# Kernel optimization log

Hardware: AMD Instinct MI355X
Metric: run time of the kernel (lower is better)

The kernel has to match this reference:

```python
import jax, jax.numpy as jnp
import numpy as np

N_NODES = 2048
EMBED = 256
STATE = 128
HID = 256
N_ACT = 256
TEAMS = 8
PAIR_F = 14


def setup_inputs() -> dict:
    key = jax.random.key(0)
    ks = jax.random.split(key, 12)
    B, T = 16, 32
    node_embeddings = jax.random.normal(ks[0], (N_NODES, EMBED), jnp.float32)
    states = jax.random.normal(ks[1], (B, T, STATE), jnp.float32)
    pair_features = jax.random.normal(ks[2], (B, T, N_ACT, PAIR_F), jnp.float32)
    proc_action_indices = jax.random.randint(ks[3], (N_ACT,), 0, N_NODES)
    in_dim = EMBED * 4 + PAIR_F
    s = lambda k, sh, fan: jax.random.normal(k, sh, jnp.float32) / np.sqrt(fan)
    return {
        "node_embeddings": node_embeddings,
        "states": states,
        "pair_features": pair_features,
        "proc_action_indices": proc_action_indices,
        "team_table": jax.random.normal(ks[4], (TEAMS, EMBED), jnp.float32),
        "Ws": s(ks[5], (STATE, EMBED), STATE),
        "bs": jnp.zeros((EMBED,), jnp.float32),
        "W1": s(ks[6], (in_dim, HID), in_dim),
        "b1": jnp.zeros((HID,), jnp.float32),
        "W2": s(ks[7], (HID, HID), HID),
        "b2": jnp.zeros((HID,), jnp.float32),
        "W3": s(ks[8], (HID, 1), HID),
        "b3": jnp.zeros((1,), jnp.float32),
    }


def reference(node_embeddings, states, pair_features, proc_action_indices,
              team_table, Ws, bs, W1, b1, W2, b2, W3, b3):
    B, T, A, F = pair_features.shape
    team_ids = jnp.arange(A) % TEAMS  # registered buffer
    # [A, E] gathered / per-action embeddings
    proc_emb = node_embeddings[proc_action_indices]          # [A, E]
    team_emb = team_table[team_ids]                          # [A, E]
    global_emb = jnp.mean(node_embeddings, axis=0)           # [E]
    state_emb = jax.nn.relu(states @ Ws + bs)                # [B, T, E]
    # broadcast + concat -> [B, T, A, 4E + F]
    bT = (B, T, A)
    scorer_input = jnp.concatenate([
        jnp.broadcast_to(proc_emb[None, None], bT + (proc_emb.shape[-1],)),
        jnp.broadcast_to(team_emb[None, None], bT + (team_emb.shape[-1],)),
        jnp.broadcast_to(global_emb[None, None, None], bT + (global_emb.shape[-1],)),
        jnp.broadcast_to(state_emb[:, :, None], bT + (state_emb.shape[-1],)),
        pair_features,
    ], axis=-1)
    h = jax.nn.relu(scorer_input @ W1 + b1)
    h = jax.nn.relu(h @ W2 + b2)
    scores = (h @ W3 + b3)[..., 0]  # [B, T, A]
    return scores[:, :, None, :]    # [B, T, 1, A]
```

## Files before the change

kernel.cpp:

```cpp
#include <hip/hip_runtime.h>
#include <hip/hip_bf16.h>

#define N_NODES 2048
#define EMBED 256
#define STATE 128
#define HID 256
#define N_ACT 256
#define TEAMS 8
#define PAIR_F 14
#define BT_TOTAL 512
#define M_TOTAL (BT_TOTAL * N_ACT)

typedef _Float16 f16_t;
typedef _Float16 f16x8 __attribute__((ext_vector_type(8)));
typedef _Float16 f16x4 __attribute__((ext_vector_type(4)));
typedef _Float16 f16x2 __attribute__((ext_vector_type(2)));
typedef float f32x4 __attribute__((ext_vector_type(4)));

__device__ __forceinline__ size_t reord_idx(int k, int n, int KB) {
    return (size_t)(((n >> 4) * KB + (k >> 5)) * 4 + ((k >> 3) & 3)) * 128 +
           (size_t)(n & 15) * 8 + (k & 7);
}

__device__ __forceinline__ size_t par_idx(int a, int n) {
    return (size_t)(a >> 4) * 4096 + (size_t)(n >> 2) * 64 + (a & 15) * 4 + (n & 3);
}

__device__ __forceinline__ f16x8 gather8(const float* __restrict__ W, int k0, int n, int ld) {
    f16x8 r;
#pragma unroll
    for (int j = 0; j < 8; ++j) r[j] = (f16_t)W[(size_t)(k0 + j) * ld + n];
    return r;
}

__device__ __forceinline__ f16x2 pk_relu(f16x2 x) {
    f16x2 r;
    asm("v_pk_max_f16 %0, %1, %2" : "=v"(r) : "v"(x), "v"(f16x2{(_Float16)0, (_Float16)0}));
    return r;
}

__device__ __forceinline__ f16x2 cvt_pk(float lo, float hi) {
    return __builtin_bit_cast(f16x2, __builtin_amdgcn_cvt_pkrtz(lo, hi));
}

__global__ void k_prep(const float* __restrict__ ne, const int* __restrict__ idx,
                       const float* __restrict__ team, const float* __restrict__ states,
                       const float* __restrict__ Ws, const float* __restrict__ W1,
                       const float* __restrict__ W2, const float* __restrict__ pf,
                       float* __restrict__ gpart, f16_t* __restrict__ vecs,
                       f16_t* __restrict__ W1abT, f16_t* __restrict__ W1cT,
                       f16_t* __restrict__ W1dT, f16_t* __restrict__ WsT,
                       f16_t* __restrict__ W2s, f16_t* __restrict__ w1pt,
                       f16_t* __restrict__ states_h, f16_t* __restrict__ pf16) {
    int bid = blockIdx.x;
    if (bid < 64) {
        int t = threadIdx.x;
        float s = 0.f;
        const float* base = ne + (size_t)bid * 32 * EMBED + t;
#pragma unroll
        for (int i = 0; i < 32; ++i) s += base[(size_t)i * EMBED];
        gpart[bid * EMBED + t] = s;
        return;
    }
    int u = (bid - 64) * 256 + threadIdx.x;
    if (u < 16384) {
        int a = u >> 6, e = (u & 63) * 8;
        f16x8 r;
        if (e < 256) {
            const float* src = ne + (size_t)idx[a] * EMBED + e;
#pragma unroll
            for (int j = 0; j < 8; ++j) r[j] = (f16_t)src[j];
        } else {
            const float* src = team + (size_t)(a % TEAMS) * EMBED + (e - 256);
#pragma unroll
            for (int j = 0; j < 8; ++j) r[j] = (f16_t)src[j];
        }
        *(f16x8*)(vecs + (size_t)u * 8) = r;
        return;
    }
    u -= 16384;
    if (u < 16384) {
        int c = u & 15, q = (u >> 4) & 3, kb = (u >> 6) & 15, g = u >> 10;
        *(f16x8*)(W1abT + (size_t)u * 8) = gather8(W1, kb * 32 + q * 8, g * 16 + c, HID);
        return;
    }
    u -= 16384;
    if (u < 8192) {
        int c = u & 15, q = (u >> 4) & 3, kb = (u >> 6) & 7, g = u >> 9;
        *(f16x8*)(W1cT + (size_t)u * 8) = gather8(W1, 512 + kb * 32 + q * 8, g * 16 + c, HID);
        return;
    }
    u -= 8192;
    if (u < 8192) {
        int c = u & 15, q = (u >> 4) & 3, kb = (u >> 6) & 7, g = u >> 9;
        *(f16x8*)(W1dT + (size_t)u * 8) = gather8(W1, 768 + kb * 32 + q * 8, g * 16 + c, HID);
        return;
    }
    u -= 8192;
    if (u < 4096) {
        int c = u & 15, q = (u >> 4) & 3, kb = (u >> 6) & 3, g = u >> 8;
        *(f16x8*)(WsT + (size_t)u * 8) = gather8(Ws, kb * 32 + q * 8, g * 16 + c, EMBED);
        return;
    }
    u -= 4096;
    if (u < 8192) {
        int c = u & 15, q = (u >> 4) & 3, kb = (u >> 6) & 7, g = u >> 9;
        *(f16x8*)(W2s + (size_t)u * 8) = gather8(W2, kb * 32 + q * 8, g * 16 + c, HID);
        return;
    }
    u -= 8192;
    if (u < 1024) {
        int c = u & 15, q = (u >> 4) & 3, g = u >> 6;
        int n = g * 16 + c, k0 = q * 8;
        f16x8 r;
#pragma unroll
        for (int j = 0; j < 8; ++j) {
            int k = k0 + j;
            r[j] = (f16_t)((k < PAIR_F) ? W1[(size_t)(1024 + k) * HID + n] : 0.f);
        }
        *(f16x8*)(w1pt + (size_t)u * 8) = r;
        return;
    }
    u -= 1024;
    if (u < 8192) {
        const float* src = states + (size_t)u * 8;
        f16x8 r;
#pragma unroll
        for (int j = 0; j < 8; ++j) r[j] = (f16_t)src[j];
        *(f16x8*)(states_h + (size_t)u * 8) = r;
        return;
    }
    u -= 8192;
    if (u < 262144) {
        int m = u >> 1, h = u & 1;
        const float* row = pf + (size_t)m * PAIR_F;
        f16x8 r;
        if (h == 0) {
#pragma unroll
            for (int j = 0; j < 4; ++j) {
                float2 v = *(const float2*)(row + j * 2);
                r[j * 2] = (f16_t)v.x; r[j * 2 + 1] = (f16_t)v.y;
            }
        } else {
#pragma unroll
            for (int j = 0; j < 3; ++j) {
                float2 v = *(const float2*)(row + 8 + j * 2);
                r[j * 2] = (f16_t)v.x; r[j * 2 + 1] = (f16_t)v.y;
            }
            r[6] = (f16_t)0.f; r[7] = (f16_t)0.f;
        }
        *(f16x8*)(pf16 + (size_t)u * 8) = r;
    }
}

__global__ __launch_bounds__(256, 4) void k_pp(
    const f16_t* __restrict__ states_h, const f16_t* __restrict__ WsT,
    const float* __restrict__ bs, const f16_t* __restrict__ W1dT,
    const f16_t* __restrict__ vecs, const f16_t* __restrict__ W1abT,
    const f16_t* __restrict__ W1cT, const float* __restrict__ gpart,
    const float* __restrict__ b1, f16_t* __restrict__ paR,
    f16_t* __restrict__ pbt_h) {
    __shared__ __align__(16) f16_t se[32 * 256];
    __shared__ __align__(16) f16_t gml[256];
    const int tid = threadIdx.x;
    const int wid = tid >> 6, lane = tid & 63;
    const int c = lane & 15, q = lane >> 4;
    int bid = blockIdx.x;

    if (bid >= 16) {
        {
            float s = 0.f;
#pragma unroll 8
            for (int p = 0; p < 64; ++p) s += gpart[p * EMBED + tid];
            gml[tid] = (f16_t)(s * (1.0f / N_NODES));
        }
        __syncthreads();
        int b = bid - 16;
        const int m0 = (b >> 2) * 32, n0 = (b & 3) * 64;
        const int n = n0 + wid * 16 + c;
        const int g = n >> 4;
        f32x4 acc[2] = {f32x4{0,0,0,0}, f32x4{0,0,0,0}};
        for (int ks = 0; ks < 16; ++ks) {
            f16x8 bf = *(const f16x8*)(W1abT + (size_t)((g * 16 + ks) * 4 + q) * 128 + c * 8);
#pragma unroll
            for (int mi = 0; mi < 2; ++mi) {
                f16x8 af = *(const f16x8*)(vecs + (size_t)(m0 + mi * 16 + c) * 512 + ks * 32 + q * 8);
                acc[mi] = __builtin_amdgcn_mfma_f32_16x16x32_f16(af, bf, acc[mi], 0, 0, 0);
            }
        }
#pragma unroll
        for (int ks = 0; ks < 8; ++ks) {
            f16x8 bf = *(const f16x8*)(W1cT + (size_t)((g * 8 + ks) * 4 + q) * 128 + c * 8);
            f16x8 af = *(const f16x8*)(gml + ks * 32 + q * 8);
#pragma unroll
            for (int mi = 0; mi < 2; ++mi)
                acc[mi] = __builtin_amdgcn_mfma_f32_16x16x32_f16(af, bf, acc[mi], 0, 0, 0);
        }
        float b1v = b1[n];
#pragma unroll
        for (int mi = 0; mi < 2; ++mi)
#pragma unroll
            for (int j = 0; j < 4; ++j) {
                int a = m0 + mi * 16 + q * 4 + j;
                paR[par_idx(a, n)] = (f16_t)(acc[mi][j] + b1v);
            }
        return;
    }

    const int bt0 = bid * 32;
    f32x4 acc[2][4];
#pragma unroll
    for (int mi = 0; mi < 2; ++mi)
#pragma unroll
        for (int ni = 0; ni < 4; ++ni) acc[mi][ni] = f32x4{0, 0, 0, 0};
#pragma unroll
    for (int ks = 0; ks < 4; ++ks) {
        f16x8 bh[4];
#pragma unroll
        for (int ni = 0; ni < 4; ++ni) {
            int g = wid * 4 + ni;
            bh[ni] = *(const f16x8*)(WsT + (size_t)((g * 4 + ks) * 4 + q) * 128 + c * 8);
        }
#pragma unroll
        for (int mi = 0; mi < 2; ++mi) {
            f16x8 af = *(const f16x8*)(states_h + (size_t)(bt0 + mi * 16 + c) * STATE + ks * 32 + q * 8);
#pragma unroll
            for (int ni = 0; ni < 4; ++ni)
                acc[mi][ni] = __builtin_amdgcn_mfma_f32_16x16x32_f16(af, bh[ni], acc[mi][ni], 0, 0, 0);
        }
    }
#pragma unroll
    for (int mi = 0; mi < 2; ++mi)
#pragma unroll
        for (int ni = 0; ni < 4; ++ni) {
            float bsv = bs[wid * 64 + ni * 16 + c];
#pragma unroll
            for (int j = 0; j < 4; ++j) {
                int m = mi * 16 + q * 4 + j;
                int n = wid * 64 + ni * 16 + c;
                se[m * 256 + (n ^ ((m & 7) << 3))] = (f16_t)fmaxf(acc[mi][ni][j] + bsv, 0.f);
            }
        }
#pragma unroll
    for (int mi = 0; mi < 2; ++mi)
#pragma unroll
        for (int ni = 0; ni < 4; ++ni) acc[mi][ni] = f32x4{0, 0, 0, 0};
    __syncthreads();
#pragma unroll
    for (int ks = 0; ks < 8; ++ks) {
        f16x8 bh[4];
#pragma unroll
        for (int ni = 0; ni < 4; ++ni) {
            int g = wid * 4 + ni;
            bh[ni] = *(const f16x8*)(W1dT + (size_t)((g * 8 + ks) * 4 + q) * 128 + c * 8);
        }
#pragma unroll
        for (int mi = 0; mi < 2; ++mi) {
            int m = mi * 16 + c;
            f16x8 ah = *(const f16x8*)(&se[m * 256 + ((ks * 32 + q * 8) ^ ((m & 7) << 3))]);
#pragma unroll
            for (int ni = 0; ni < 4; ++ni)
                acc[mi][ni] = __builtin_amdgcn_mfma_f32_16x16x32_f16(ah, bh[ni], acc[mi][ni], 0, 0, 0);
        }
    }
#pragma unroll
    for (int mi = 0; mi < 2; ++mi)
#pragma unroll
        for (int ni = 0; ni < 4; ++ni)
#pragma unroll
            for (int j = 0; j < 4; ++j)
                pbt_h[(size_t)(bt0 + mi * 16 + q * 4 + j) * HID + wid * 64 + ni * 16 + c] =
                    (f16_t)acc[mi][ni][j];
}

__global__ __launch_bounds__(512, 4) void k_main(
    const f16_t* __restrict__ pf16, const f16_t* __restrict__ paR,
    const f16_t* __restrict__ pbt, const f16_t* __restrict__ w2s,
    const f16_t* __restrict__ w1pt, const float* __restrict__ b2,
    const float* __restrict__ W3, const float* __restrict__ b3,
    float* __restrict__ out) {
    __shared__ __align__(16) f16_t Ah[128 * 256];
    __shared__ float red[4][128];

    const int tid = threadIdx.x;
    const int wid = tid >> 6, lane = tid & 63;
    const int wr = wid >> 2, wc = wid & 3;
    const int c = lane & 15, q = lane >> 4;

    const int r0 = blockIdx.x * 128;
    const int bt = r0 >> 8;
    const int a0 = r0 & 255;

    f32x4 acc[16];
#pragma unroll
    for (int i = 0; i < 16; ++i) acc[i] = f32x4{0, 0, 0, 0};

    f16x4 pbtv[4];
#pragma unroll
    for (int nf = 0; nf < 4; ++nf)
        pbtv[nf] = *(const f16x4*)(pbt + (size_t)bt * HID + wc * 64 + nf * 16 + q * 4);

    f16x8 af[4];
#pragma unroll
    for (int nf = 0; nf < 4; ++nf) {
        int g = wc * 4 + nf;
        af[nf] = *(const f16x8*)(w1pt + (size_t)(g * 4 + q) * 128 + c * 8);
    }

    f16x4 pavA[4], pavB[4];
    {
        int n0 = wc * 64 + 0 * 16 + q * 4;
#pragma unroll
        for (int mf = 0; mf < 4; ++mf)
            pavA[mf] = *(const f16x4*)(paR + (size_t)((a0 >> 4) + wr * 4 + mf) * 4096 +
                                       (size_t)(n0 >> 2) * 64 + c * 4);
    }

#pragma unroll
    for (int mf = 0; mf < 4; ++mf) {
        int m = wr * 64 + mf * 16 + c;
        f16x8 bf;
        if (q < 2) bf = *(const f16x8*)(pf16 + (size_t)(r0 + m) * 16 + q * 8);
        else bf = f16x8{(_Float16)0, (_Float16)0, (_Float16)0, (_Float16)0,
                        (_Float16)0, (_Float16)0, (_Float16)0, (_Float16)0};
        __builtin_amdgcn_s_setprio(1);
#pragma unroll
        for (int nf = 0; nf < 4; ++nf)
            acc[nf * 4 + mf] = __builtin_amdgcn_mfma_f32_16x16x32_f16(af[nf], bf, acc[nf * 4 + mf], 0, 0, 0);
        __builtin_amdgcn_s_setprio(0);
    }

#pragma unroll
    for (int nf = 0; nf < 4; ++nf) {
        if (nf < 3) {
            int n1 = wc * 64 + (nf + 1) * 16 + q * 4;
#pragma unroll
            for (int mf = 0; mf < 4; ++mf)
                pavB[mf] = *(const f16x4*)(paR + (size_t)((a0 >> 4) + wr * 4 + mf) * 4096 +
                                           (size_t)(n1 >> 2) * 64 + c * 4);
        }
        int n0 = wc * 64 + nf * 16 + q * 4;
        f16x2 pb01 = {pbtv[nf][0], pbtv[nf][1]}, pb23 = {pbtv[nf][2], pbtv[nf][3]};
#pragma unroll
        for (int mf = 0; mf < 4; ++mf) {
            int m = wr * 64 + mf * 16 + c;
            f16x2 pa01 = {pavA[mf][0], pavA[mf][1]}, pa23 = {pavA[mf][2], pavA[mf][3]};
            f32x4 a = acc[nf * 4 + mf];
            f16x2 h01 = cvt_pk(a[0], a[1]);
            f16x2 h23 = cvt_pk(a[2], a[3]);
            h01 = pk_relu(h01 + pa01 + pb01);
            h23 = pk_relu(h23 + pa23 + pb23);
            f16x4 hv = __builtin_shufflevector(h01, h23, 0, 1, 2, 3);
            *(f16x4*)(&Ah[m * 256 + (n0 ^ ((m & 7) << 3))]) = hv;
        }
#pragma unroll
        for (int mf = 0; mf < 4; ++mf) pavA[mf] = pavB[mf];
    }

#pragma unroll
    for (int i = 0; i < 16; ++i) acc[i] = f32x4{0, 0, 0, 0};

    f16x8 bh[4];
#pragma unroll
    for (int ni = 0; ni < 4; ++ni) {
        int g = wc * 4 + ni;
        bh[ni] = *(const f16x8*)(w2s + (size_t)((g * 8 + 0) * 4 + q) * 128 + c * 8);
    }

    __syncthreads();

#pragma unroll
    for (int ks = 0; ks < 8; ++ks) {
        f16x8 bhn[4];
        if (ks < 7) {
#pragma unroll
            for (int ni = 0; ni < 4; ++ni) {
                int g = wc * 4 + ni;
                bhn[ni] = *(const f16x8*)(w2s + (size_t)((g * 8 + ks + 1) * 4 + q) * 128 + c * 8);
            }
        }
        f16x8 ahA, ahB;
        {
            int m = wr * 64 + 0 * 16 + c;
            ahA = *(const f16x8*)(&Ah[m * 256 + ((ks * 32 + q * 8) ^ ((m & 7) << 3))]);
        }
        __builtin_amdgcn_s_setprio(1);
#pragma unroll
        for (int mi = 0; mi < 4; ++mi) {
            if (mi < 3) {
                int m1 = wr * 64 + (mi + 1) * 16 + c;
                ahB = *(const f16x8*)(&Ah[m1 * 256 + ((ks * 32 + q * 8) ^ ((m1 & 7) << 3))]);
            }
#pragma unroll
            for (int ni = 0; ni < 4; ++ni)
                acc[mi * 4 + ni] = __builtin_amdgcn_mfma_f32_16x16x32_f16(ahA, bh[ni], acc[mi * 4 + ni], 0, 0, 0);
            ahA = ahB;
        }
        __builtin_amdgcn_s_setprio(0);
#pragma unroll
        for (int ni = 0; ni < 4; ++ni) bh[ni] = bhn[ni];
    }

    float p[4][4];
#pragma unroll
    for (int mi = 0; mi < 4; ++mi)
#pragma unroll
        for (int j = 0; j < 4; ++j) p[mi][j] = 0.f;
#pragma unroll
    for (int ni = 0; ni < 4; ++ni) {
        int n = wc * 64 + ni * 16 + c;
        float b2v = b2[n];
        float w3v = W3[n];
#pragma unroll
        for (int mi = 0; mi < 4; ++mi)
#pragma unroll
            for (int j = 0; j < 4; ++j)
                p[mi][j] = fmaf(fmaxf(acc[mi * 4 + ni][j] + b2v, 0.f), w3v, p[mi][j]);
    }
#pragma unroll
    for (int off = 1; off < 16; off <<= 1)
#pragma unroll
        for (int mi = 0; mi < 4; ++mi)
#pragma unroll
            for (int j = 0; j < 4; ++j) p[mi][j] += __shfl_xor(p[mi][j], off, 64);

    if (c == 0) {
#pragma unroll
        for (int mi = 0; mi < 4; ++mi)
#pragma unroll
            for (int j = 0; j < 4; ++j) red[wc][wr * 64 + mi * 16 + q * 4 + j] = p[mi][j];
    }
    __syncthreads();

    if (tid < 128) {
        out[(size_t)r0 + tid] = red[0][tid] + red[1][tid] + red[2][tid] + red[3][tid] + b3[0];
    }
}

extern "C" void kernel_launch(void* const* d_in, const int* in_sizes, int n_in,
                              void* d_out, int out_size, void* d_ws, size_t ws_size,
                              hipStream_t stream) {
    (void)in_sizes; (void)n_in; (void)out_size; (void)ws_size;
    const float* ne     = (const float*)d_in[0];
    const float* states = (const float*)d_in[1];
    const float* pf     = (const float*)d_in[2];
    const int*   idx    = (const int*)d_in[3];
    const float* team   = (const float*)d_in[4];
    const float* Ws     = (const float*)d_in[5];
    const float* bs     = (const float*)d_in[6];
    const float* W1     = (const float*)d_in[7];
    const float* b1     = (const float*)d_in[8];
    const float* W2     = (const float*)d_in[9];
    const float* b2     = (const float*)d_in[10];
    const float* W3     = (const float*)d_in[11];
    const float* b3     = (const float*)d_in[12];
    float* out = (float*)d_out;

    char* ws = (char*)d_ws;
    float* gpart    = (float*)(ws + 0);
    f16_t* vecs     = (f16_t*)(ws + 65536);
    f16_t* W1abT    = (f16_t*)(ws + 327680);
    f16_t* W1cT     = (f16_t*)(ws + 589824);
    f16_t* W1dT     = (f16_t*)(ws + 720896);
    f16_t* WsT      = (f16_t*)(ws + 851968);
    f16_t* W2s      = (f16_t*)(ws + 917504);
    f16_t* w1pt     = (f16_t*)(ws + 1048576);
    f16_t* states_h = (f16_t*)(ws + 1064960);
    f16_t* paR      = (f16_t*)(ws + 1196032);
    f16_t* pbt_h    = (f16_t*)(ws + 1327104);
    f16_t* pf16     = (f16_t*)(ws + 1589248);

    k_prep<<<64 + 1300, 256, 0, stream>>>(ne, idx, team, states, Ws, W1, W2, pf,
                                          gpart, vecs, W1abT, W1cT, W1dT, WsT, W2s,
                                          w1pt, states_h, pf16);
    k_pp<<<48, 256, 0, stream>>>(states_h, WsT, bs, W1dT, vecs, W1abT, W1cT,
                                 gpart, b1, paR, pbt_h);
    k_main<<<M_TOTAL / 128, 512, 0, stream>>>(pf16, paR, pbt_h, W2s, w1pt, b2, W3, b3, out);
}
```

Baseline: 42.93 us.

## Fuse prep and projection kernels into one launch reading fp32 inputs directly

Merges the prep and per-action/per-state projection kernels into a single kernel. The projection blocks now read fp32 embeddings, states and weights directly and convert inline, instead of using pre-converted fp16 buffers. Each pa block computes the global mean over all nodes itself. This removes a kernel launch and intermediate workspace traffic, at the cost of redundant mean reduction and uncoalesced weight gathers on the critical path.

Result: slower. 80.93 us (+88.5%).

```diff
diff --git a/kernel.cpp b/kernel.cpp
--- a/kernel.cpp
+++ b/kernel.cpp
@@ -17,11 +17,6 @@
 typedef _Float16 f16x2 __attribute__((ext_vector_type(2)));
 typedef float f32x4 __attribute__((ext_vector_type(4)));
 
-__device__ __forceinline__ size_t reord_idx(int k, int n, int KB) {
-    return (size_t)(((n >> 4) * KB + (k >> 5)) * 4 + ((k >> 3) & 3)) * 128 +
-           (size_t)(n & 15) * 8 + (k & 7);
-}
-
 __device__ __forceinline__ size_t par_idx(int a, int n) {
     return (size_t)(a >> 4) * 4096 + (size_t)(n >> 2) * 64 + (a & 15) * 4 + (n & 3);
 }
@@ -30,6 +25,14 @@
     f16x8 r;
 #pragma unroll
     for (int j = 0; j < 8; ++j) r[j] = (f16_t)W[(size_t)(k0 + j) * ld + n];
+    return r;
+}
+
+__device__ __forceinline__ f16x8 load8_f32(const float* __restrict__ p) {
+    float4 v0 = *(const float4*)p, v1 = *(const float4*)(p + 4);
+    f16x8 r;
+    r[0] = (f16_t)v0.x; r[1] = (f16_t)v0.y; r[2] = (f16_t)v0.z; r[3] = (f16_t)v0.w;
+    r[4] = (f16_t)v1.x; r[5] = (f16_t)v1.y; r[6] = (f16_t)v1.z; r[7] = (f16_t)v1.w;
     return r;
 }
 
@@ -43,123 +46,15 @@
     return __builtin_bit_cast(f16x2, __builtin_amdgcn_cvt_pkrtz(lo, hi));
 }
 
-__global__ void k_prep(const float* __restrict__ ne, const int* __restrict__ idx,
-                       const float* __restrict__ team, const float* __restrict__ states,
-                       const float* __restrict__ Ws, const float* __restrict__ W1,
-                       const float* __restrict__ W2, const float* __restrict__ pf,
-                       float* __restrict__ gpart, f16_t* __restrict__ vecs,
-                       f16_t* __restrict__ W1abT, f16_t* __restrict__ W1cT,
-                       f16_t* __restrict__ W1dT, f16_t* __restrict__ WsT,
-                       f16_t* __restrict__ W2s, f16_t* __restrict__ w1pt,
-                       f16_t* __restrict__ states_h, f16_t* __restrict__ pf16) {
-    int bid = blockIdx.x;
-    if (bid < 64) {
-        int t = threadIdx.x;
-        float s = 0.f;
-        const float* base = ne + (size_t)bid * 32 * EMBED + t;
-#pragma unroll
-        for (int i = 0; i < 32; ++i) s += base[(size_t)i * EMBED];
-        gpart[bid * EMBED + t] = s;
-        return;
-    }
-    int u = (bid - 64) * 256 + threadIdx.x;
-    if (u < 16384) {
-        int a = u >> 6, e = (u & 63) * 8;
-        f16x8 r;
-        if (e < 256) {
-            const float* src = ne + (size_t)idx[a] * EMBED + e;
-#pragma unroll
-            for (int j = 0; j < 8; ++j) r[j] = (f16_t)src[j];
-        } else {
-            const float* src = team + (size_t)(a % TEAMS) * EMBED + (e - 256);
-#pragma unroll
-            for (int j = 0; j < 8; ++j) r[j] = (f16_t)src[j];
-        }
-        *(f16x8*)(vecs + (size_t)u * 8) = r;
-        return;
-    }
-    u -= 16384;
-    if (u < 16384) {
-        int c = u & 15, q = (u >> 4) & 3, kb = (u >> 6) & 15, g = u >> 10;
-        *(f16x8*)(W1abT + (size_t)u * 8) = gather8(W1, kb * 32 + q * 8, g * 16 + c, HID);
-        return;
-    }
-    u -= 16384;
-    if (u < 8192) {
-        int c = u & 15, q = (u >> 4) & 3, kb = (u >> 6) & 7, g = u >> 9;
-        *(f16x8*)(W1cT + (size_t)u * 8) = gather8(W1, 512 + kb * 32 + q * 8, g * 16 + c, HID);
-        return;
-    }
-    u -= 8192;
-    if (u < 8192) {
-        int c = u & 15, q = (u >> 4) & 3, kb = (u >> 6) & 7, g = u >> 9;
-        *(f16x8*)(W1dT + (size_t)u * 8) = gather8(W1, 768 + kb * 32 + q * 8, g * 16 + c, HID);
-        return;
-    }
-    u -= 8192;
-    if (u < 4096) {
-        int c = u & 15, q = (u >> 4) & 3, kb = (u >> 6) & 3, g = u >> 8;
-        *(f16x8*)(WsT + (size_t)u * 8) = gather8(Ws, kb * 32 + q * 8, g * 16 + c, EMBED);
-        return;
-    }
-    u -= 4096;
-    if (u < 8192) {
-        int c = u & 15, q = (u >> 4) & 3, kb = (u >> 6) & 7, g = u >> 9;
-        *(f16x8*)(W2s + (size_t)u * 8) = gather8(W2, kb * 32 + q * 8, g * 16 + c, HID);
-        return;
-    }
-    u -= 8192;
-    if (u < 1024) {
-        int c = u & 15, q = (u >> 4) & 3, g = u >> 6;
-        int n = g * 16 + c, k0 = q * 8;
-        f16x8 r;
-#pragma unroll
-        for (int j = 0; j < 8; ++j) {
-            int k = k0 + j;
-            r[j] = (f16_t)((k < PAIR_F) ? W1[(size_t)(1024 + k) * HID + n] : 0.f);
-        }
-        *(f16x8*)(w1pt + (size_t)u * 8) = r;
-        return;
-    }
-    u -= 1024;
-    if (u < 8192) {
-        const float* src = states + (size_t)u * 8;
-        f16x8 r;
-#pragma unroll
-        for (int j = 0; j < 8; ++j) r[j] = (f16_t)src[j];
-        *(f16x8*)(states_h + (size_t)u * 8) = r;
-        return;
-    }
-    u -= 8192;
-    if (u < 262144) {
-        int m = u >> 1, h = u & 1;
-        const float* row = pf + (size_t)m * PAIR_F;
-        f16x8 r;
-        if (h == 0) {
-#pragma unroll
-            for (int j = 0; j < 4; ++j) {
-                float2 v = *(const float2*)(row + j * 2);
-                r[j * 2] = (f16_t)v.x; r[j * 2 + 1] = (f16_t)v.y;
-            }
-        } else {
-#pragma unroll
-            for (int j = 0; j < 3; ++j) {
-                float2 v = *(const float2*)(row + 8 + j * 2);
-                r[j * 2] = (f16_t)v.x; r[j * 2 + 1] = (f16_t)v.y;
-            }
-            r[6] = (f16_t)0.f; r[7] = (f16_t)0.f;
-        }
-        *(f16x8*)(pf16 + (size_t)u * 8) = r;
-    }
-}
-
-__global__ __launch_bounds__(256, 4) void k_pp(
-    const f16_t* __restrict__ states_h, const f16_t* __restrict__ WsT,
-    const float* __restrict__ bs, const f16_t* __restrict__ W1dT,
-    const f16_t* __restrict__ vecs, const f16_t* __restrict__ W1abT,
-    const f16_t* __restrict__ W1cT, const float* __restrict__ gpart,
-    const float* __restrict__ b1, f16_t* __restrict__ paR,
-    f16_t* __restrict__ pbt_h) {
+__global__ __launch_bounds__(256, 4) void k_all(
+    const float* __restrict__ ne, const int* __restrict__ idx,
+    const float* __restrict__ team, const float* __restrict__ states,
+    const float* __restrict__ Ws, const float* __restrict__ W1,
+    const float* __restrict__ W2, const float* __restrict__ pf,
+    const float* __restrict__ bs, const float* __restrict__ b1,
+    f16_t* __restrict__ W2s, f16_t* __restrict__ w1pt,
+    f16_t* __restrict__ paR, f16_t* __restrict__ pbt_h,
+    f16_t* __restrict__ pf16) {
     __shared__ __align__(16) f16_t se[32 * 256];
     __shared__ __align__(16) f16_t gml[256];
     const int tid = threadIdx.x;
@@ -167,110 +62,166 @@
     const int c = lane & 15, q = lane >> 4;
     int bid = blockIdx.x;
 
-    if (bid >= 16) {
-        {
-            float s = 0.f;
-#pragma unroll 8
-            for (int p = 0; p < 64; ++p) s += gpart[p * EMBED + tid];
-            gml[tid] = (f16_t)(s * (1.0f / N_NODES));
-        }
+    if (bid < 48) {
+        if (bid >= 16) {
+            {
+                float s0 = 0, s1 = 0, s2 = 0, s3 = 0, s4 = 0, s5 = 0, s6 = 0, s7 = 0;
+                const float* col = ne + tid;
+                for (int r = 0; r < N_NODES; r += 8) {
+                    s0 += col[(size_t)(r + 0) * EMBED]; s1 += col[(size_t)(r + 1) * EMBED];
+                    s2 += col[(size_t)(r + 2) * EMBED]; s3 += col[(size_t)(r + 3) * EMBED];
+                    s4 += col[(size_t)(r + 4) * EMBED]; s5 += col[(size_t)(r + 5) * EMBED];
+                    s6 += col[(size_t)(r + 6) * EMBED]; s7 += col[(size_t)(r + 7) * EMBED];
+                }
+                float s = ((s0 + s1) + (s2 + s3)) + ((s4 + s5) + (s6 + s7));
+                gml[tid] = (f16_t)(s * (1.0f / N_NODES));
+            }
+            __syncthreads();
+            int b = bid - 16;
+            const int m0 = (b >> 2) * 32, n0 = (b & 3) * 64;
+            const int n = n0 + wid * 16 + c;
+            f32x4 acc[2] = {f32x4{0, 0, 0, 0}, f32x4{0, 0, 0, 0}};
+            const float* neb[2];
+            const float* tmb[2];
+#pragma unroll
+            for (int mi = 0; mi < 2; ++mi) {
+                int m = m0 + mi * 16 + c;
+                neb[mi] = ne + (size_t)idx[m] * EMBED;
+                tmb[mi] = team + (size_t)(m % TEAMS) * EMBED;
+            }
+#pragma unroll
+            for (int ks = 0; ks < 16; ++ks) {
+                f16x8 bf = gather8(W1, ks * 32 + q * 8, n, HID);
+#pragma unroll
+                for (int mi = 0; mi < 2; ++mi) {
+                    int e0 = ks * 32 + q * 8;
+                    const float* src = (ks < 8) ? (neb[mi] + e0) : (tmb[mi] + (e0 - 256));
+                    f16x8 af = load8_f32(src);
+                    acc[mi] = __builtin_amdgcn_mfma_f32_16x16x32_f16(af, bf, acc[mi], 0, 0, 0);
+                }
+            }
+#pragma unroll
+            for (int ks = 0; ks < 8; ++ks) {
+                f16x8 bf = gather8(W1, 512 + ks * 32 + q * 8, n, HID);
+                f16x8 af = *(const f16x8*)(gml + ks * 32 + q * 8);
+#pragma unroll
+                for (int mi = 0; mi < 2; ++mi)
+                    acc[mi] = __builtin_amdgcn_mfma_f32_16x16x32_f16(af, bf, acc[mi], 0, 0, 0);
+            }
+            float b1v = b1[n];
+#pragma unroll
+            for (int mi = 0; mi < 2; ++mi)
+#pragma unroll
+                for (int j = 0; j < 4; ++j) {
+                    int a = m0 + mi * 16 + q * 4 + j;
+                    paR[par_idx(a, n)] = (f16_t)(acc[mi][j] + b1v);
+                }
+            return;
+        }
+
+        const int bt0 = bid * 32;
+        f32x4 acc[2][4];
+#pragma unroll
+        for (int mi = 0; mi < 2; ++mi)
+#pragma unroll
+            for (int ni = 0; ni < 4; ++ni) acc[mi][ni] = f32x4{0, 0, 0, 0};
+#pragma unroll
+        for (int ks = 0; ks < 4; ++ks) {
+            f16x8 bh[4];
+#pragma unroll
+            for (int ni = 0; ni < 4; ++ni)
+                bh[ni] = gather8(Ws, ks * 32 + q * 8, (wid * 4 + ni) * 16 + c, EMBED);
+#pragma unroll
+            for (int mi = 0; mi < 2; ++mi) {
+                f16x8 af = load8_f32(states + (size_t)(bt0 + mi * 16 + c) * STATE + ks * 32 + q * 8);
+#pragma unroll
+                for (int ni = 0; ni < 4; ++ni)
+                    acc[mi][ni] = __builtin_amdgcn_mfma_f32_16x16x32_f16(af, bh[ni], acc[mi][ni], 0, 0, 0);
+            }
+        }
+#pragma unroll
+        for (int mi = 0; mi < 2; ++mi)
+#pragma unroll
+            for (int ni = 0; ni < 4; ++ni) {
+                float bsv = bs[wid * 64 + ni * 16 + c];
+#pragma unroll
+                for (int j = 0; j < 4; ++j) {
+                    int m = mi * 16 + q * 4 + j;
+                    int n = wid * 64 + ni * 16 + c;
+                    se[m * 256 + (n ^ ((m & 7) << 3))] = (f16_t)fmaxf(acc[mi][ni][j] + bsv, 0.f);
+                }
+            }
+#pragma unroll
+        for (int mi = 0; mi < 2; ++mi)
+#pragma unroll
+            for (int ni = 0; ni < 4; ++ni) acc[mi][ni] = f32x4{0, 0, 0, 0};
         __syncthreads();
-        int b = bid - 16;
-        const int m0 = (b >> 2) * 32, n0 = (b & 3) * 64;
-        const int n = n0 + wid * 16 + c;
-        const int g = n >> 4;
-        f32x4 acc[2] = {f32x4{0,0,0,0}, f32x4{0,0,0,0}};
-        for (int ks = 0; ks < 16; ++ks) {
-            f16x8 bf = *(const f16x8*)(W1abT + (size_t)((g * 16 + ks) * 4 + q) * 128 + c * 8);
+#pragma unroll
+        for (int ks = 0; ks < 8; ++ks) {
+            f16x8 bh[4];
+#pragma unroll
+            for (int ni = 0; ni < 4; ++ni)
+                bh[ni] = gather8(W1, 768 + ks * 32 + q * 8, (wid * 4 + ni) * 16 + c, HID);
 #pragma unroll
             for (int mi = 0; mi < 2; ++mi) {
-                f16x8 af = *(const f16x8*)(vecs + (size_t)(m0 + mi * 16 + c) * 512 + ks * 32 + q * 8);
-                acc[mi] = __builtin_amdgcn_mfma_f32_16x16x32_f16(af, bf, acc[mi], 0, 0, 0);
-            }
-        }
-#pragma unroll
-        for (int ks = 0; ks < 8; ++ks) {
-            f16x8 bf = *(const f16x8*)(W1cT + (size_t)((g * 8 + ks) * 4 + q) * 128 + c * 8);
-            f16x8 af = *(const f16x8*)(gml + ks * 32 + q * 8);
-#pragma unroll
-            for (int mi = 0; mi < 2; ++mi)
-                acc[mi] = __builtin_amdgcn_mfma_f32_16x16x32_f16(af, bf, acc[mi], 0, 0, 0);
-        }
-        float b1v = b1[n];
+                int m = mi * 16 + c;
+                f16x8 ah = *(const f16x8*)(&se[m * 256 + ((ks * 32 + q * 8) ^ ((m & 7) << 3))]);
+#pragma unroll
+                for (int ni = 0; ni < 4; ++ni)
+                    acc[mi][ni] = __builtin_amdgcn_mfma_f32_16x16x32_f16(ah, bh[ni], acc[mi][ni], 0, 0, 0);
+            }
+        }
 #pragma unroll
         for (int mi = 0; mi < 2; ++mi)
 #pragma unroll
+            for (int ni = 0; ni < 4; ++ni)
+#pragma unroll
+                for (int j = 0; j < 4; ++j)
+                    pbt_h[(size_t)(bt0 + mi * 16 + q * 4 + j) * HID + wid * 64 + ni * 16 + c] =
+                        (f16_t)acc[mi][ni][j];
+        return;
+    }
+
+    int u = (bid - 48) * 256 + tid;
+    if (u < 262144) {
+        int m = u >> 1, h = u & 1;
+        const float* row = pf + (size_t)m * PAIR_F;
+        f16x8 r;
+        if (h == 0) {
+#pragma unroll
             for (int j = 0; j < 4; ++j) {
-                int a = m0 + mi * 16 + q * 4 + j;
-                paR[par_idx(a, n)] = (f16_t)(acc[mi][j] + b1v);
-            }
+                float2 v = *(const float2*)(row + j * 2);
+                r[j * 2] = (f16_t)v.x; r[j * 2 + 1] = (f16_t)v.y;
+            }
+        } else {
+#pragma unroll
+            for (int j = 0; j < 3; ++j) {
+                float2 v = *(const float2*)(row + 8 + j * 2);
+                r[j * 2] = (f16_t)v.x; r[j * 2 + 1] = (f16_t)v.y;
+            }
+            r[6] = (f16_t)0.f; r[7] = (f16_t)0.f;
+        }
+        *(f16x8*)(pf16 + (size_t)u * 8) = r;
         return;
     }
-
-    const int bt0 = bid * 32;
-    f32x4 acc[2][4];
-#pragma unroll
-    for (int mi = 0; mi < 2; ++mi)
-#pragma unroll
-        for (int ni = 0; ni < 4; ++ni) acc[mi][ni] = f32x4{0, 0, 0, 0};
-#pragma unroll
-    for (int ks = 0; ks < 4; ++ks) {
-        f16x8 bh[4];
-#pragma unroll
-        for (int ni = 0; ni < 4; ++ni) {
-            int g = wid * 4 + ni;
-            bh[ni] = *(const f16x8*)(WsT + (size_t)((g * 4 + ks) * 4 + q) * 128 + c * 8);
-        }
-#pragma unroll
-        for (int mi = 0; mi < 2; ++mi) {
-            f16x8 af = *(const f16x8*)(states_h + (size_t)(bt0 + mi * 16 + c) * STATE + ks * 32 + q * 8);
-#pragma unroll
-            for (int ni = 0; ni < 4; ++ni)
-                acc[mi][ni] = __builtin_amdgcn_mfma_f32_16x16x32_f16(af, bh[ni], acc[mi][ni], 0, 0, 0);
-        }
-    }
-#pragma unroll
-    for (int mi = 0; mi < 2; ++mi)
-#pragma unroll
-        for (int ni = 0; ni < 4; ++ni) {
-            float bsv = bs[wid * 64 + ni * 16 + c];
-#pragma unroll
-            for (int j = 0; j < 4; ++j) {
-                int m = mi * 16 + q * 4 + j;
-                int n = wid * 64 + ni * 16 + c;
-                se[m * 256 + (n ^ ((m & 7) << 3))] = (f16_t)fmaxf(acc[mi][ni][j] + bsv, 0.f);
-            }
-        }
-#pragma unroll
-    for (int mi = 0; mi < 2; ++mi)
-#pragma unroll
-        for (int ni = 0; ni < 4; ++ni) acc[mi][ni] = f32x4{0, 0, 0, 0};
-    __syncthreads();
-#pragma unroll
-    for (int ks = 0; ks < 8; ++ks) {
-        f16x8 bh[4];
-#pragma unroll
-        for (int ni = 0; ni < 4; ++ni) {
-            int g = wid * 4 + ni;
-            bh[ni] = *(const f16x8*)(W1dT + (size_t)((g * 8 + ks) * 4 + q) * 128 + c * 8);
-        }
-#pragma unroll
-        for (int mi = 0; mi < 2; ++mi) {
-            int m = mi * 16 + c;
-            f16x8 ah = *(const f16x8*)(&se[m * 256 + ((ks * 32 + q * 8) ^ ((m & 7) << 3))]);
-#pragma unroll
-            for (int ni = 0; ni < 4; ++ni)
-                acc[mi][ni] = __builtin_amdgcn_mfma_f32_16x16x32_f16(ah, bh[ni], acc[mi][ni], 0, 0, 0);
-        }
-    }
-#pragma unroll
-    for (int mi = 0; mi < 2; ++mi)
-#pragma unroll
-        for (int ni = 0; ni < 4; ++ni)
-#pragma unroll
-            for (int j = 0; j < 4; ++j)
-                pbt_h[(size_t)(bt0 + mi * 16 + q * 4 + j) * HID + wid * 64 + ni * 16 + c] =
-                    (f16_t)acc[mi][ni][j];
+    u -= 262144;
+    if (u < 8192) {
+        int c2 = u & 15, q2 = (u >> 4) & 3, kb = (u >> 6) & 7, g = u >> 9;
+        *(f16x8*)(W2s + (size_t)u * 8) = gather8(W2, kb * 32 + q2 * 8, g * 16 + c2, HID);
+        return;
+    }
+    u -= 8192;
+    if (u < 1024) {
+        int c2 = u & 15, q2 = (u >> 4) & 3, g = u >> 6;
+        int n = g * 16 + c2, k0 = q2 * 8;
+        f16x8 r;
+#pragma unroll
+        for (int j = 0; j < 8; ++j) {
+            int k = k0 + j;
+            r[j] = (f16_t)((k < PAIR_F) ? W1[(size_t)(1024 + k) * HID + n] : 0.f);
+        }
+        *(f16x8*)(w1pt + (size_t)u * 8) = r;
+    }
 }
 
 __global__ __launch_bounds__(512, 4) void k_main(
@@ -457,23 +408,13 @@
     float* out = (float*)d_out;
 
     char* ws = (char*)d_ws;
-    float* gpart    = (float*)(ws + 0);
-    f16_t* vecs     = (f16_t*)(ws + 65536);
-    f16_t* W1abT    = (f16_t*)(ws + 327680);
-    f16_t* W1cT     = (f16_t*)(ws + 589824);
-    f16_t* W1dT     = (f16_t*)(ws + 720896);
-    f16_t* WsT      = (f16_t*)(ws + 851968);
-    f16_t* W2s      = (f16_t*)(ws + 917504);
-    f16_t* w1pt     = (f16_t*)(ws + 1048576);
-    f16_t* states_h = (f16_t*)(ws + 1064960);
-    f16_t* paR      = (f16_t*)(ws + 1196032);
-    f16_t* pbt_h    = (f16_t*)(ws + 1327104);
-    f16_t* pf16     = (f16_t*)(ws + 1589248);
-
-    k_prep<<<64 + 1300, 256, 0, stream>>>(ne, idx, team, states, Ws, W1, W2, pf,
-                                          gpart, vecs, W1abT, W1cT, W1dT, WsT, W2s,
-                                          w1pt, states_h, pf16);
-    k_pp<<<48, 256, 0, stream>>>(states_h, WsT, bs, W1dT, vecs, W1abT, W1cT,
-                                 gpart, b1, paR, pbt_h);
+    f16_t* W2s   = (f16_t*)(ws + 0);
+    f16_t* w1pt  = (f16_t*)(ws + 131072);
+    f16_t* paR   = (f16_t*)(ws + 147456);
+    f16_t* pbt_h = (f16_t*)(ws + 278528);
+    f16_t* pf16  = (f16_t*)(ws + 540672);
+
+    k_all<<<48 + 1060, 256, 0, stream>>>(ne, idx, team, states, Ws, W1, W2, pf,
+                                         bs, b1, W2s, w1pt, paR, pbt_h, pf16);
     k_main<<<M_TOTAL / 128, 512, 0, stream>>>(pf16, paR, pbt_h, W2s, w1pt, b2, W3, b3, out);
 }
```

## Move pair-feature and W2 conversion into the precompute kernel to overlap work

Applied to the files above, without the earlier changes.

Splits the preparation work differently across the two pre-kernels. The first kernel now only does what the small precompute GEMMs depend on (global sum, gathers, W1/Ws transposes, states conversion). The large pair-feature f16 conversion and the W2/w1p repacking move into the second kernel, where they run alongside the 48 MFMA precompute blocks. This shortens the critical path before the precompute GEMMs and fills the GPU during the otherwise tiny 48-block launch. In exchange, the second kernel carries a larger shared-memory and register footprint for all its blocks.

Result: no change. 42.78 us, median of 3 (-0.3%).

```diff
diff --git a/kernel.cpp b/kernel.cpp
--- a/kernel.cpp
+++ b/kernel.cpp
@@ -17,11 +17,6 @@
 typedef _Float16 f16x2 __attribute__((ext_vector_type(2)));
 typedef float f32x4 __attribute__((ext_vector_type(4)));
 
-__device__ __forceinline__ size_t reord_idx(int k, int n, int KB) {
-    return (size_t)(((n >> 4) * KB + (k >> 5)) * 4 + ((k >> 3) & 3)) * 128 +
-           (size_t)(n & 15) * 8 + (k & 7);
-}
-
 __device__ __forceinline__ size_t par_idx(int a, int n) {
     return (size_t)(a >> 4) * 4096 + (size_t)(n >> 2) * 64 + (a & 15) * 4 + (n & 3);
 }
@@ -43,15 +38,13 @@
     return __builtin_bit_cast(f16x2, __builtin_amdgcn_cvt_pkrtz(lo, hi));
 }
 
-__global__ void k_prep(const float* __restrict__ ne, const int* __restrict__ idx,
-                       const float* __restrict__ team, const float* __restrict__ states,
-                       const float* __restrict__ Ws, const float* __restrict__ W1,
-                       const float* __restrict__ W2, const float* __restrict__ pf,
-                       float* __restrict__ gpart, f16_t* __restrict__ vecs,
-                       f16_t* __restrict__ W1abT, f16_t* __restrict__ W1cT,
-                       f16_t* __restrict__ W1dT, f16_t* __restrict__ WsT,
-                       f16_t* __restrict__ W2s, f16_t* __restrict__ w1pt,
-                       f16_t* __restrict__ states_h, f16_t* __restrict__ pf16) {
+__global__ void k_prepA(const float* __restrict__ ne, const int* __restrict__ idx,
+                        const float* __restrict__ team, const float* __restrict__ states,
+                        const float* __restrict__ Ws, const float* __restrict__ W1,
+                        float* __restrict__ gpart, f16_t* __restrict__ vecs,
+                        f16_t* __restrict__ W1abT, f16_t* __restrict__ W1cT,
+                        f16_t* __restrict__ W1dT, f16_t* __restrict__ WsT,
+                        f16_t* __restrict__ states_h) {
     int bid = blockIdx.x;
     if (bid < 64) {
         int t = threadIdx.x;
@@ -104,62 +97,24 @@
     }
     u -= 4096;
     if (u < 8192) {
-        int c = u & 15, q = (u >> 4) & 3, kb = (u >> 6) & 7, g = u >> 9;
-        *(f16x8*)(W2s + (size_t)u * 8) = gather8(W2, kb * 32 + q * 8, g * 16 + c, HID);
-        return;
-    }
-    u -= 8192;
-    if (u < 1024) {
-        int c = u & 15, q = (u >> 4) & 3, g = u >> 6;
-        int n = g * 16 + c, k0 = q * 8;
-        f16x8 r;
-#pragma unroll
-        for (int j = 0; j < 8; ++j) {
-            int k = k0 + j;
-            r[j] = (f16_t)((k < PAIR_F) ? W1[(size_t)(1024 + k) * HID + n] : 0.f);
-        }
-        *(f16x8*)(w1pt + (size_t)u * 8) = r;
-        return;
-    }
-    u -= 1024;
-    if (u < 8192) {
         const float* src = states + (size_t)u * 8;
         f16x8 r;
 #pragma unroll
         for (int j = 0; j < 8; ++j) r[j] = (f16_t)src[j];
         *(f16x8*)(states_h + (size_t)u * 8) = r;
-        return;
-    }
-    u -= 8192;
-    if (u < 262144) {
-        int m = u >> 1, h = u & 1;
-        const float* row = pf + (size_t)m * PAIR_F;
-        f16x8 r;
-        if (h == 0) {
-#pragma unroll
-            for (int j = 0; j < 4; ++j) {
-                float2 v = *(const float2*)(row + j * 2);
-                r[j * 2] = (f16_t)v.x; r[j * 2 + 1] = (f16_t)v.y;
-            }
-        } else {
-#pragma unroll
-            for (int j = 0; j < 3; ++j) {
-                float2 v = *(const float2*)(row + 8 + j * 2);
-                r[j * 2] = (f16_t)v.x; r[j * 2 + 1] = (f16_t)v.y;
-            }
-            r[6] = (f16_t)0.f; r[7] = (f16_t)0.f;
-        }
-        *(f16x8*)(pf16 + (size_t)u * 8) = r;
-    }
-}
-
-__global__ __launch_bounds__(256, 4) void k_pp(
-    const f16_t* __restrict__ states_h, const f16_t* __restrict__ WsT,
-    const float* __restrict__ bs, const f16_t* __restrict__ W1dT,
-    const f16_t* __restrict__ vecs, const f16_t* __restrict__ W1abT,
-    const f16_t* __restrict__ W1cT, const float* __restrict__ gpart,
-    const float* __restrict__ b1, f16_t* __restrict__ paR,
-    f16_t* __restrict__ pbt_h) {
+    }
+}
+
+__global__ __launch_bounds__(256, 4) void k_prepB(
+    const float* __restrict__ pf, const float* __restrict__ W1,
+    const float* __restrict__ W2, const f16_t* __restrict__ states_h,
+    const f16_t* __restrict__ WsT, const float* __restrict__ bs,
+    const f16_t* __restrict__ W1dT, const f16_t* __restrict__ vecs,
+    const f16_t* __restrict__ W1abT, const f16_t* __restrict__ W1cT,
+    const float* __restrict__ gpart, const float* __restrict__ b1,
+    f16_t* __restrict__ W2s, f16_t* __restrict__ w1pt,
+    f16_t* __restrict__ paR, f16_t* __restrict__ pbt_h,
+    f16_t* __restrict__ pf16) {
     __shared__ __align__(16) f16_t se[32 * 256];
     __shared__ __align__(16) f16_t gml[256];
     const int tid = threadIdx.x;
@@ -167,110 +122,154 @@
     const int c = lane & 15, q = lane >> 4;
     int bid = blockIdx.x;
 
-    if (bid >= 16) {
-        {
-            float s = 0.f;
+    if (bid < 48) {
+        if (bid >= 16) {
+            {
+                float s = 0.f;
 #pragma unroll 8
-            for (int p = 0; p < 64; ++p) s += gpart[p * EMBED + tid];
-            gml[tid] = (f16_t)(s * (1.0f / N_NODES));
-        }
+                for (int p = 0; p < 64; ++p) s += gpart[p * EMBED + tid];
+                gml[tid] = (f16_t)(s * (1.0f / N_NODES));
+            }
+            __syncthreads();
+            int b = bid - 16;
+            const int m0 = (b >> 2) * 32, n0 = (b & 3) * 64;
+            const int n = n0 + wid * 16 + c;
+            const int g = n >> 4;
+            f32x4 acc[2] = {f32x4{0, 0, 0, 0}, f32x4{0, 0, 0, 0}};
+            for (int ks = 0; ks < 16; ++ks) {
+                f16x8 bf = *(const f16x8*)(W1abT + (size_t)((g * 16 + ks) * 4 + q) * 128 + c * 8);
+#pragma unroll
+                for (int mi = 0; mi < 2; ++mi) {
+                    f16x8 af = *(const f16x8*)(vecs + (size_t)(m0 + mi * 16 + c) * 512 + ks * 32 + q * 8);
+                    acc[mi] = __builtin_amdgcn_mfma_f32_16x16x32_f16(af, bf, acc[mi], 0, 0, 0);
+                }
+            }
+#pragma unroll
+            for (int ks = 0; ks < 8; ++ks) {
+                f16x8 bf = *(const f16x8*)(W1cT + (size_t)((g * 8 + ks) * 4 + q) * 128 + c * 8);
+                f16x8 af = *(const f16x8*)(gml + ks * 32 + q * 8);
+#pragma unroll
+                for (int mi = 0; mi < 2; ++mi)
+                    acc[mi] = __builtin_amdgcn_mfma_f32_16x16x32_f16(af, bf, acc[mi], 0, 0, 0);
+            }
+            float b1v = b1[n];
+#pragma unroll
+            for (int mi = 0; mi < 2; ++mi)
+#pragma unroll
+                for (int j = 0; j < 4; ++j) {
+                    int a = m0 + mi * 16 + q * 4 + j;
+                    paR[par_idx(a, n)] = (f16_t)(acc[mi][j] + b1v);
+                }
+            return;
+        }
+
+        const int bt0 = bid * 32;
+        f32x4 acc[2][4];
+#pragma unroll
+        for (int mi = 0; mi < 2; ++mi)
+#pragma unroll
+            for (int ni = 0; ni < 4; ++ni) acc[mi][ni] = f32x4{0, 0, 0, 0};
+#pragma unroll
+        for (int ks = 0; ks < 4; ++ks) {
+            f16x8 bh[4];
+#pragma unroll
+            for (int ni = 0; ni < 4; ++ni) {
+                int g = wid * 4 + ni;
+                bh[ni] = *(const f16x8*)(WsT + (size_t)((g * 4 + ks) * 4 + q) * 128 + c * 8);
+            }
+#pragma unroll
+            for (int mi = 0; mi < 2; ++mi) {
+                f16x8 af = *(const f16x8*)(states_h + (size_t)(bt0 + mi * 16 + c) * STATE + ks * 32 + q * 8);
+#pragma unroll
+                for (int ni = 0; ni < 4; ++ni)
+                    acc[mi][ni] = __builtin_amdgcn_mfma_f32_16x16x32_f16(af, bh[ni], acc[mi][ni], 0, 0, 0);
+            }
+        }
+#pragma unroll
+        for (int mi = 0; mi < 2; ++mi)
+#pragma unroll
+            for (int ni = 0; ni < 4; ++ni) {
+                float bsv = bs[wid * 64 + ni * 16 + c];
+#pragma unroll
+                for (int j = 0; j < 4; ++j) {
+                    int m = mi * 16 + q * 4 + j;
+                    int n = wid * 64 + ni * 16 + c;
+                    se[m * 256 + (n ^ ((m & 7) << 3))] = (f16_t)fmaxf(acc[mi][ni][j] + bsv, 0.f);
+                }
+            }
+#pragma unroll
+        for (int mi = 0; mi < 2; ++mi)
+#pragma unroll
+            for (int ni = 0; ni < 4; ++ni) acc[mi][ni] = f32x4{0, 0, 0, 0};
         __syncthreads();
-        int b = bid - 16;
-        const int m0 = (b >> 2) * 32, n0 = (b & 3) * 64;
-        const int n = n0 + wid * 16 + c;
-        const int g = n >> 4;
-        f32x4 acc[2] = {f32x4{0,0,0,0}, f32x4{0,0,0,0}};
-        for (int ks = 0; ks < 16; ++ks) {
-            f16x8 bf = *(const f16x8*)(W1abT + (size_t)((g * 16 + ks) * 4 + q) * 128 + c * 8);
+#pragma unroll
+        for (int ks = 0; ks < 8; ++ks) {
+            f16x8 bh[4];
+#pragma unroll
+            for (int ni = 0; ni < 4; ++ni) {
+                int g = wid * 4 + ni;
+                bh[ni] = *(const f16x8*)(W1dT + (size_t)((g * 8 + ks) * 4 + q) * 128 + c * 8);
+            }
 #pragma unroll
             for (int mi = 0; mi < 2; ++mi) {
-                f16x8 af = *(const f16x8*)(vecs + (size_t)(m0 + mi * 16 + c) * 512 + ks * 32 + q * 8);
-                acc[mi] = __builtin_amdgcn_mfma_f32_16x16x32_f16(af, bf, acc[mi], 0, 0, 0);
-            }
-        }
-#pragma unroll
-        for (int ks = 0; ks < 8; ++ks) {
-            f16x8 bf = *(const f16x8*)(W1cT + (size_t)((g * 8 + ks) * 4 + q) * 128 + c * 8);
-            f16x8 af = *(const f16x8*)(gml + ks * 32 + q * 8);
-#pragma unroll
-            for (int mi = 0; mi < 2; ++mi)
-                acc[mi] = __builtin_amdgcn_mfma_f32_16x16x32_f16(af, bf, acc[mi], 0, 0, 0);
-        }
-        float b1v = b1[n];
+                int m = mi * 16 + c;
+                f16x8 ah = *(const f16x8*)(&se[m * 256 + ((ks * 32 + q * 8) ^ ((m & 7) << 3))]);
+#pragma unroll
+                for (int ni = 0; ni < 4; ++ni)
+                    acc[mi][ni] = __builtin_amdgcn_mfma_f32_16x16x32_f16(ah, bh[ni], acc[mi][ni], 0, 0, 0);
+            }
+        }
 #pragma unroll
         for (int mi = 0; mi < 2; ++mi)
 #pragma unroll
+            for (int ni = 0; ni < 4; ++ni)
+#pragma unroll
+                for (int j = 0; j < 4; ++j)
+                    pbt_h[(size_t)(bt0 + mi * 16 + q * 4 + j) * HID + wid * 64 + ni * 16 + c] =
+                        (f16_t)acc[mi][ni][j];
+        return;
+    }
+
+    int u = (bid - 48) * 256 + tid;
+    if (u < 262144) {
+        int m = u >> 1, h = u & 1;
+        const float* row = pf + (size_t)m * PAIR_F;
+        f16x8 r;
+        if (h == 0) {
+#pragma unroll
             for (int j = 0; j < 4; ++j) {
-                int a = m0 + mi * 16 + q * 4 + j;
-                paR[par_idx(a, n)] = (f16_t)(acc[mi][j] + b1v);
-            }
-        return;
-    }
-
-    const int bt0 = bid * 32;
-    f32x4 acc[2][4];
-#pragma unroll
-    for (int mi = 0; mi < 2; ++mi)
-#pragma unroll
-        for (int ni = 0; ni < 4; ++ni) acc[mi][ni] = f32x4{0, 0, 0, 0};
-#pragma unroll
-    for (int ks = 0; ks < 4; ++ks) {
-        f16x8 bh[4];
-#pragma unroll
-        for (int ni = 0; ni < 4; ++ni) {
-            int g = wid * 4 + ni;
-            bh[ni] = *(const f16x8*)(WsT + (size_t)((g * 4 + ks) * 4 + q) * 128 + c * 8);
-        }
-#pragma unroll
-        for (int mi = 0; mi < 2; ++mi) {
-            f16x8 af = *(const f16x8*)(states_h + (size_t)(bt0 + mi * 16 + c) * STATE + ks * 32 + q * 8);
-#pragma unroll
-            for (int ni = 0; ni < 4; ++ni)
-                acc[mi][ni] = __builtin_amdgcn_mfma_f32_16x16x32_f16(af, bh[ni], acc[mi][ni], 0, 0, 0);
-        }
-    }
-#pragma unroll
-    for (int mi = 0; mi < 2; ++mi)
-#pragma unroll
-        for (int ni = 0; ni < 4; ++ni) {
-            float bsv = bs[wid * 64 + ni * 16 + c];
-#pragma unroll
-            for (int j = 0; j < 4; ++j) {
-                int m = mi * 16 + q * 4 + j;
-                int n = wid * 64 + ni * 16 + c;
-                se[m * 256 + (n ^ ((m & 7) << 3))] = (f16_t)fmaxf(acc[mi][ni][j] + bsv, 0.f);
-            }
-        }
-#pragma unroll
-    for (int mi = 0; mi < 2; ++mi)
-#pragma unroll
-        for (int ni = 0; ni < 4; ++ni) acc[mi][ni] = f32x4{0, 0, 0, 0};
-    __syncthreads();
-#pragma unroll
-    for (int ks = 0; ks < 8; ++ks) {
-        f16x8 bh[4];
-#pragma unroll
-        for (int ni = 0; ni < 4; ++ni) {
-            int g = wid * 4 + ni;
-            bh[ni] = *(const f16x8*)(W1dT + (size_t)((g * 8 + ks) * 4 + q) * 128 + c * 8);
-        }
-#pragma unroll
-        for (int mi = 0; mi < 2; ++mi) {
-            int m = mi * 16 + c;
-            f16x8 ah = *(const f16x8*)(&se[m * 256 + ((ks * 32 + q * 8) ^ ((m & 7) << 3))]);
-#pragma unroll
-            for (int ni = 0; ni < 4; ++ni)
-                acc[mi][ni] = __builtin_amdgcn_mfma_f32_16x16x32_f16(ah, bh[ni], acc[mi][ni], 0, 0, 0);
-        }
-    }
-#pragma unroll
-    for (int mi = 0; mi < 2; ++mi)
-#pragma unroll
-        for (int ni = 0; ni < 4; ++ni)
-#pragma unroll
-            for (int j = 0; j < 4; ++j)
-                pbt_h[(size_t)(bt0 + mi * 16 + q * 4 + j) * HID + wid * 64 + ni * 16 + c] =
-                    (f16_t)acc[mi][ni][j];
+                float2 v = *(const float2*)(row + j * 2);
+                r[j * 2] = (f16_t)v.x; r[j * 2 + 1] = (f16_t)v.y;
+            }
+        } else {
+#pragma unroll
+            for (int j = 0; j < 3; ++j) {
+                float2 v = *(const float2*)(row + 8 + j * 2);
+                r[j * 2] = (f16_t)v.x; r[j * 2 + 1] = (f16_t)v.y;
+            }
+            r[6] = (f16_t)0.f; r[7] = (f16_t)0.f;
+        }
+        *(f16x8*)(pf16 + (size_t)u * 8) = r;
+        return;
+    }
+    u -= 262144;
+    if (u < 8192) {
+        int c2 = u & 15, q2 = (u >> 4) & 3, kb = (u >> 6) & 7, g = u >> 9;
+        *(f16x8*)(W2s + (size_t)u * 8) = gather8(W2, kb * 32 + q2 * 8, g * 16 + c2, HID);
+        return;
+    }
+    u -= 8192;
+    if (u < 1024) {
+        int c2 = u & 15, q2 = (u >> 4) & 3, g = u >> 6;
+        int n = g * 16 + c2, k0 = q2 * 8;
+        f16x8 r;
+#pragma unroll
+        for (int j = 0; j < 8; ++j) {
+            int k = k0 + j;
+            r[j] = (f16_t)((k < PAIR_F) ? W1[(size_t)(1024 + k) * HID + n] : 0.f);
+        }
+        *(f16x8*)(w1pt + (size_t)u * 8) = r;
+    }
 }
 
 __global__ __launch_bounds__(512, 4) void k_main(
@@ -470,10 +469,10 @@
     f16_t* pbt_h    = (f16_t*)(ws + 1327104);
     f16_t* pf16     = (f16_t*)(ws + 1589248);
 
-    k_prep<<<64 + 1300, 256, 0, stream>>>(ne, idx, team, states, Ws, W1, W2, pf,
-                                          gpart, vecs, W1abT, W1cT, W1dT, WsT, W2s,
-                                          w1pt, states_h, pf16);
-    k_pp<<<48, 256, 0, stream>>>(states_h, WsT, bs, W1dT, vecs, W1abT, W1cT,
-                                 gpart, b1, paR, pbt_h);
+    k_prepA<<<64 + 240, 256, 0, stream>>>(ne, idx, team, states, Ws, W1,
+                                          gpart, vecs, W1abT, W1cT, W1dT, WsT, states_h);
+    k_prepB<<<48 + 1060, 256, 0, stream>>>(pf, W1, W2, states_h, WsT, bs, W1dT,
+                                           vecs, W1abT, W1cT, gpart, b1,
+                                           W2s, w1pt, paR, pbt_h, pf16);
     k_main<<<M_TOTAL / 128, 512, 0, stream>>>(pf16, paR, pbt_h, W2s, w1pt, b2, W3, b3, out);
 }
```
